# Kernel optimization log

Measured on AMD Instinct MI355X. Metric: run time of the kernel, lower is better.

## Reference

```python
import jax, jax.numpy as jnp
import numpy as np

HOP_NUM = 3
N_NODES = 40000
N_EDGES = 640000
IN_DIM = 128
N_ALPHAS = HOP_NUM * (HOP_NUM + 1) // 2  # triangular layerRegular params


def setup_inputs() -> dict:
    key = jax.random.key(0)
    k_h, k_d, k_a, k_s, k_t = jax.random.split(key, 5)
    h = jax.random.normal(k_h, (N_NODES, IN_DIM), dtype=jnp.float32)
    d = jax.random.uniform(k_d, (N_NODES,), dtype=jnp.float32)  # degree normalization per node
    alphas = jax.random.uniform(k_a, (N_ALPHAS,), dtype=jnp.float32)
    src = jax.random.randint(k_s, (N_EDGES,), 0, N_NODES, dtype=jnp.int32)
    dst = jax.random.randint(k_t, (N_EDGES,), 0, N_NODES, dtype=jnp.int32)
    return {"h": h, "d": d, "alphas": alphas, "src": src, "dst": dst}


def reference(h, d, alphas, src, dst):
    n = h.shape[0]
    # edge_applying: e = 1 * d[dst] * d[src]  (symmetric-normalized edge weight)
    e = d[dst] * d[src]                      # [E]
    outs = [h]
    k = 0
    for i in range(HOP_NUM):
        feat = h
        for q in range(i + 1):
            # update_all(u_mul_e('h','e'), sum): agg[v] = sum_{(u,v)} feat[u] * e
            msg = feat[src] * e[:, None]     # [E, D]
            agg = jax.ops.segment_sum(msg, dst, num_segments=n)  # [N, D]
            a = alphas[k]; k += 1
            feat = agg * a + (1.0 - a) * feat
            # feature_drop with p=0.0 (eval) is identity
        outs.append(feat)
    return jnp.concatenate(outs, axis=1)       # [N, (HOP_NUM+1)*D]
```

## Files before the change

kernel.cpp:

```cpp
#include <hip/hip_runtime.h>


#define NN  40000
#define NE  640000
#define CAP 64

__device__ inline unsigned short f2h(float f) {
    _Float16 h = (_Float16)f;
    return *(unsigned short*)&h;
}
__device__ inline float h2f(unsigned short u) {
    _Float16 h = *(_Float16*)&u;
    return (float)h;
}
__device__ inline unsigned short f2bf(float f) {
    unsigned int x = __float_as_uint(f);
    x += 0x7fffu + ((x >> 16) & 1u);
    return (unsigned short)(x >> 16);
}
__device__ inline unsigned int pack_bf2(float x, float y) {
    return ((unsigned int)f2bf(y) << 16) | (unsigned int)f2bf(x);
}
__device__ inline float bflo(unsigned int u) { return __uint_as_float(u << 16); }
__device__ inline float bfhi(unsigned int u) { return __uint_as_float(u & 0xffff0000u); }

__global__ __launch_bounds__(256) void build_cvt_k(
    const int* __restrict__ src, const int* __restrict__ dst,
    const float* __restrict__ deg, const float* __restrict__ h,
    int* __restrict__ counts, unsigned int* __restrict__ buck,
    unsigned int* __restrict__ hb) {
    int b = blockIdx.x;
    if (b < NE / 256) {
        int e = b * 256 + threadIdx.x;
        int s = src[e];
        int v = dst[e];
        int slot = atomicAdd(&counts[v], 1);
        if (slot < CAP) {
            float w = deg[s] * deg[v];
            buck[v * CAP + slot] = ((unsigned int)f2h(w) << 16) | (unsigned int)s;
        }
    } else {
        int i = (b - NE / 256) * 256 + threadIdx.x;
        if (i < NN * 64) {
            float2 f = *(const float2*)(h + (size_t)i * 2);
            hb[i] = pack_bf2(f.x, f.y);
        }
    }
}

__device__ inline float2 gather_node(
    const unsigned int* __restrict__ feat,
    const int* __restrict__ counts, const unsigned int* __restrict__ buck,
    int v, int lane) {
    int vs = __builtin_amdgcn_readfirstlane(v);
    int cnt = counts[vs];
    if (cnt > CAP) cnt = CAP;
    const unsigned int* brow = buck + (size_t)vs * CAP;

    float ax = 0.f, ay = 0.f, bx = 0.f, by = 0.f;
    float cx = 0.f, cy = 0.f, dx = 0.f, dy = 0.f;
    for (int j = 0; j < cnt; j += 8) {
        unsigned int uu[8];
#pragma unroll
        for (int k = 0; k < 8; ++k) uu[k] = brow[j + k];
        float wj[8]; int sj[8];
#pragma unroll
        for (int k = 0; k < 8; ++k) {
            bool ok = (j + k) < cnt;
            wj[k] = ok ? h2f((unsigned short)(uu[k] >> 16)) : 0.f;
            sj[k] = ok ? (int)(uu[k] & 0xffffu) : 0;
        }
        unsigned int fj[8];
#pragma unroll
        for (int k = 0; k < 8; ++k)
            fj[k] = feat[(size_t)sj[k] * 64 + lane];
#pragma unroll
        for (int k = 0; k < 8; k += 4) {
            ax = fmaf(wj[k + 0], bflo(fj[k + 0]), ax);
            ay = fmaf(wj[k + 0], bfhi(fj[k + 0]), ay);
            bx = fmaf(wj[k + 1], bflo(fj[k + 1]), bx);
            by = fmaf(wj[k + 1], bfhi(fj[k + 1]), by);
            cx = fmaf(wj[k + 2], bflo(fj[k + 2]), cx);
            cy = fmaf(wj[k + 2], bfhi(fj[k + 2]), cy);
            dx = fmaf(wj[k + 3], bflo(fj[k + 3]), dx);
            dy = fmaf(wj[k + 3], bfhi(fj[k + 3]), dy);
        }
    }
    return make_float2((ax + bx) + (cx + dx), (ay + by) + (cy + dy));
}

__global__ __launch_bounds__(256) void agg_k(
    const unsigned int* __restrict__ feat,
    const int* __restrict__ counts, const unsigned int* __restrict__ buck,
    unsigned int* __restrict__ outf) {
    int gid  = blockIdx.x * 256 + threadIdx.x;
    int v    = gid >> 6;
    int lane = gid & 63;
    if (v >= NN) return;
    float2 acc = gather_node(feat, counts, buck, v, lane);
    outf[(size_t)v * 64 + lane] = pack_bf2(acc.x, acc.y);
}

__global__ __launch_bounds__(256) void agg3_fused_k(
    const unsigned int* __restrict__ p2b,
    const float* __restrict__ h,
    const unsigned int* __restrict__ p1b,
    const int* __restrict__ counts, const unsigned int* __restrict__ buck,
    const float* __restrict__ alphas, float* __restrict__ out) {
    int gid  = blockIdx.x * 256 + threadIdx.x;
    int v    = gid >> 6;
    int lane = gid & 63;
    if (v >= NN) return;
    float2 p3 = gather_node(p2b, counts, buck, v, lane);

    float a0 = alphas[0], a1 = alphas[1], a2 = alphas[2];
    float a3 = alphas[3], a4 = alphas[4], a5 = alphas[5];
    float c1p = a0, c1h = 1.f - a0;
    float c2pp = a2 * a1;
    float c2p  = a2 * (1.f - a1) + (1.f - a2) * a1;
    float c2h  = (1.f - a2) * (1.f - a1);
    float s2pp = a4 * a3;
    float s2p  = a4 * (1.f - a3) + (1.f - a4) * a3;
    float s2h  = (1.f - a4) * (1.f - a3);
    float c3ppp = a5 * s2pp;
    float c3pp  = a5 * s2p + (1.f - a5) * s2pp;
    float c3p   = a5 * s2h + (1.f - a5) * s2p;
    float c3h   = (1.f - a5) * s2h;

    int i2 = lane * 2;
    float2 hf = *(const float2*)(h + (size_t)v * 128 + i2);
    unsigned int u1 = p1b[(size_t)v * 64 + lane];
    unsigned int u2 = p2b[(size_t)v * 64 + lane];
    float q1x = bflo(u1), q1y = bfhi(u1);
    float q2x = bflo(u2), q2y = bfhi(u2);

    float2 r1, r2, r3;
    r1.x = c1p * q1x + c1h * hf.x;
    r1.y = c1p * q1y + c1h * hf.y;
    r2.x = c2pp * q2x + c2p * q1x + c2h * hf.x;
    r2.y = c2pp * q2y + c2p * q1y + c2h * hf.y;
    r3.x = c3ppp * p3.x + c3pp * q2x + c3p * q1x + c3h * hf.x;
    r3.y = c3ppp * p3.y + c3pp * q2y + c3p * q1y + c3h * hf.y;

    float* o = out + (size_t)v * 512;
    *(float2*)(o + i2)       = hf;
    *(float2*)(o + 128 + i2) = r1;
    *(float2*)(o + 256 + i2) = r2;
    *(float2*)(o + 384 + i2) = r3;
}

extern "C" void kernel_launch(void* const* d_in, const int* in_sizes, int n_in,
                              void* d_out, int out_size, void* d_ws, size_t ws_size,
                              hipStream_t stream) {
    const float* h      = (const float*)d_in[0];
    const float* deg    = (const float*)d_in[1];
    const float* alphas = (const float*)d_in[2];
    const int*   src    = (const int*)d_in[3];
    const int*   dst    = (const int*)d_in[4];
    float* out = (float*)d_out;

    char* ws = (char*)d_ws;
    int*          counts = (int*)(ws + 0);
    unsigned int* buck   = (unsigned int*)(ws + 160000);
    unsigned int* hb     = (unsigned int*)(ws + 10400000);
    unsigned int* p1b    = (unsigned int*)(ws + 20640000);
    unsigned int* p2b    = (unsigned int*)(ws + 30880000);

    hipMemsetAsync(counts, 0, NN * sizeof(int), stream);
    build_cvt_k<<<NE / 256 + (NN * 64 + 255) / 256, 256, 0, stream>>>(
        src, dst, deg, h, counts, buck, hb);

    agg_k<<<NN / 4, 256, 0, stream>>>(hb,  counts, buck, p1b);
    agg_k<<<NN / 4, 256, 0, stream>>>(p1b, counts, buck, p2b);
    agg3_fused_k<<<NN / 4, 256, 0, stream>>>(p2b, h, p1b, counts, buck,
                                             alphas, out);
}
```

Measured before the change: 212.4 us.

## Merge all stages into one cooperative persistent kernel with grid syncs

Replaces the memset and the four separate launches (bucket build plus bf16 conversion, two aggregation hops, and the fused final hop) with one cooperative kernel of 1024 blocks. Grid-stride loops cover each phase, and grid.sync() separates them. The aim is to remove launch gaps and per-kernel tail effects. The cost is grid-wide barrier overhead, lower occupancy than a full launch (launch bounds 256,4), and a fixed grid that must stay co-resident for the cooperative launch to succeed.

Result: slower. 663.4 us (+212.4%).

```diff
diff --git a/kernel.cpp b/kernel.cpp
--- a/kernel.cpp
+++ b/kernel.cpp
@@ -1,76 +1,58 @@
 #include <hip/hip_runtime.h>
+#include <hip/hip_cooperative_groups.h>
 
+
+namespace cg = cooperative_groups;
 
 #define NN  40000
 #define NE  640000
 #define CAP 64
 
-__device__ inline unsigned short f2h(float f) {
+typedef unsigned int uint;
+typedef unsigned short ushort;
+
+__device__ inline ushort f2h(float f) {
     _Float16 h = (_Float16)f;
-    return *(unsigned short*)&h;
+    return *(ushort*)&h;
 }
-__device__ inline float h2f(unsigned short u) {
+__device__ inline float h2f(ushort u) {
     _Float16 h = *(_Float16*)&u;
     return (float)h;
 }
-__device__ inline unsigned short f2bf(float f) {
-    unsigned int x = __float_as_uint(f);
+__device__ inline ushort f2bf(float f) {
+    uint x = __float_as_uint(f);
     x += 0x7fffu + ((x >> 16) & 1u);
-    return (unsigned short)(x >> 16);
+    return (ushort)(x >> 16);
 }
-__device__ inline unsigned int pack_bf2(float x, float y) {
-    return ((unsigned int)f2bf(y) << 16) | (unsigned int)f2bf(x);
+__device__ inline uint pack_bf2(float x, float y) {
+    return ((uint)f2bf(y) << 16) | (uint)f2bf(x);
 }
-__device__ inline float bflo(unsigned int u) { return __uint_as_float(u << 16); }
-__device__ inline float bfhi(unsigned int u) { return __uint_as_float(u & 0xffff0000u); }
-
-__global__ __launch_bounds__(256) void build_cvt_k(
-    const int* __restrict__ src, const int* __restrict__ dst,
-    const float* __restrict__ deg, const float* __restrict__ h,
-    int* __restrict__ counts, unsigned int* __restrict__ buck,
-    unsigned int* __restrict__ hb) {
-    int b = blockIdx.x;
-    if (b < NE / 256) {
-        int e = b * 256 + threadIdx.x;
-        int s = src[e];
-        int v = dst[e];
-        int slot = atomicAdd(&counts[v], 1);
-        if (slot < CAP) {
-            float w = deg[s] * deg[v];
-            buck[v * CAP + slot] = ((unsigned int)f2h(w) << 16) | (unsigned int)s;
-        }
-    } else {
-        int i = (b - NE / 256) * 256 + threadIdx.x;
-        if (i < NN * 64) {
-            float2 f = *(const float2*)(h + (size_t)i * 2);
-            hb[i] = pack_bf2(f.x, f.y);
-        }
-    }
-}
+__device__ inline float bflo(uint u) { return __uint_as_float(u << 16); }
+__device__ inline float bfhi(uint u) { return __uint_as_float(u & 0xffff0000u); }
 
 __device__ inline float2 gather_node(
-    const unsigned int* __restrict__ feat,
-    const int* __restrict__ counts, const unsigned int* __restrict__ buck,
+    const uint* __restrict__ feat,
+    const int* __restrict__ counts, const uint* __restrict__ buck,
     int v, int lane) {
     int vs = __builtin_amdgcn_readfirstlane(v);
     int cnt = counts[vs];
     if (cnt > CAP) cnt = CAP;
-    const unsigned int* brow = buck + (size_t)vs * CAP;
+    const uint* brow = buck + (size_t)vs * CAP;
 
     float ax = 0.f, ay = 0.f, bx = 0.f, by = 0.f;
     float cx = 0.f, cy = 0.f, dx = 0.f, dy = 0.f;
     for (int j = 0; j < cnt; j += 8) {
-        unsigned int uu[8];
+        uint uu[8];
 #pragma unroll
         for (int k = 0; k < 8; ++k) uu[k] = brow[j + k];
         float wj[8]; int sj[8];
 #pragma unroll
         for (int k = 0; k < 8; ++k) {
             bool ok = (j + k) < cnt;
-            wj[k] = ok ? h2f((unsigned short)(uu[k] >> 16)) : 0.f;
+            wj[k] = ok ? h2f((ushort)(uu[k] >> 16)) : 0.f;
             sj[k] = ok ? (int)(uu[k] & 0xffffu) : 0;
         }
-        unsigned int fj[8];
+        uint fj[8];
 #pragma unroll
         for (int k = 0; k < 8; ++k)
             fj[k] = feat[(size_t)sj[k] * 64 + lane];
@@ -89,29 +71,49 @@
     return make_float2((ax + bx) + (cx + dx), (ay + by) + (cy + dy));
 }
 
-__global__ __launch_bounds__(256) void agg_k(
-    const unsigned int* __restrict__ feat,
-    const int* __restrict__ counts, const unsigned int* __restrict__ buck,
-    unsigned int* __restrict__ outf) {
-    int gid  = blockIdx.x * 256 + threadIdx.x;
-    int v    = gid >> 6;
-    int lane = gid & 63;
-    if (v >= NN) return;
-    float2 acc = gather_node(feat, counts, buck, v, lane);
-    outf[(size_t)v * 64 + lane] = pack_bf2(acc.x, acc.y);
-}
+__global__ __launch_bounds__(256, 4) void mega_k(
+    const float* __restrict__ h, const float* __restrict__ deg,
+    const float* __restrict__ alphas,
+    const int* __restrict__ src, const int* __restrict__ dst,
+    int* __restrict__ counts, uint* __restrict__ buck,
+    uint* __restrict__ hb, uint* __restrict__ p1b, uint* __restrict__ p2b,
+    float* __restrict__ out) {
+    cg::grid_group grid = cg::this_grid();
+    const int nthr = (int)(gridDim.x * 256);
+    const int tid  = (int)(blockIdx.x * 256 + threadIdx.x);
+    const int lane = tid & 63;
+    const int wid  = tid >> 6;
+    const int wstr = nthr >> 6;
 
-__global__ __launch_bounds__(256) void agg3_fused_k(
-    const unsigned int* __restrict__ p2b,
-    const float* __restrict__ h,
-    const unsigned int* __restrict__ p1b,
-    const int* __restrict__ counts, const unsigned int* __restrict__ buck,
-    const float* __restrict__ alphas, float* __restrict__ out) {
-    int gid  = blockIdx.x * 256 + threadIdx.x;
-    int v    = gid >> 6;
-    int lane = gid & 63;
-    if (v >= NN) return;
-    float2 p3 = gather_node(p2b, counts, buck, v, lane);
+    for (int i = tid; i < NN; i += nthr) counts[i] = 0;
+    grid.sync();
+
+    for (int e = tid; e < NE; e += nthr) {
+        int s = src[e];
+        int v = dst[e];
+        int slot = atomicAdd(&counts[v], 1);
+        if (slot < CAP) {
+            float w = deg[s] * deg[v];
+            buck[v * CAP + slot] = ((uint)f2h(w) << 16) | (uint)s;
+        }
+    }
+    for (int i = tid; i < NN * 64; i += nthr) {
+        float2 f = *(const float2*)(h + (size_t)i * 2);
+        hb[i] = pack_bf2(f.x, f.y);
+    }
+    grid.sync();
+
+    for (int v = wid; v < NN; v += wstr) {
+        float2 a = gather_node(hb, counts, buck, v, lane);
+        p1b[(size_t)v * 64 + lane] = pack_bf2(a.x, a.y);
+    }
+    grid.sync();
+
+    for (int v = wid; v < NN; v += wstr) {
+        float2 a = gather_node(p1b, counts, buck, v, lane);
+        p2b[(size_t)v * 64 + lane] = pack_bf2(a.x, a.y);
+    }
+    grid.sync();
 
     float a0 = alphas[0], a1 = alphas[1], a2 = alphas[2];
     float a3 = alphas[3], a4 = alphas[4], a5 = alphas[5];
@@ -127,26 +129,29 @@
     float c3p   = a5 * s2h + (1.f - a5) * s2p;
     float c3h   = (1.f - a5) * s2h;
 
-    int i2 = lane * 2;
-    float2 hf = *(const float2*)(h + (size_t)v * 128 + i2);
-    unsigned int u1 = p1b[(size_t)v * 64 + lane];
-    unsigned int u2 = p2b[(size_t)v * 64 + lane];
-    float q1x = bflo(u1), q1y = bfhi(u1);
-    float q2x = bflo(u2), q2y = bfhi(u2);
+    for (int v = wid; v < NN; v += wstr) {
+        float2 p3 = gather_node(p2b, counts, buck, v, lane);
+        int i2 = lane * 2;
+        float2 hf = *(const float2*)(h + (size_t)v * 128 + i2);
+        uint u1 = p1b[(size_t)v * 64 + lane];
+        uint u2 = p2b[(size_t)v * 64 + lane];
+        float q1x = bflo(u1), q1y = bfhi(u1);
+        float q2x = bflo(u2), q2y = bfhi(u2);
 
-    float2 r1, r2, r3;
-    r1.x = c1p * q1x + c1h * hf.x;
-    r1.y = c1p * q1y + c1h * hf.y;
-    r2.x = c2pp * q2x + c2p * q1x + c2h * hf.x;
-    r2.y = c2pp * q2y + c2p * q1y + c2h * hf.y;
-    r3.x = c3ppp * p3.x + c3pp * q2x + c3p * q1x + c3h * hf.x;
-    r3.y = c3ppp * p3.y + c3pp * q2y + c3p * q1y + c3h * hf.y;
+        float2 r1, r2, r3;
+        r1.x = c1p * q1x + c1h * hf.x;
+        r1.y = c1p * q1y + c1h * hf.y;
+        r2.x = c2pp * q2x + c2p * q1x + c2h * hf.x;
+        r2.y = c2pp * q2y + c2p * q1y + c2h * hf.y;
+        r3.x = c3ppp * p3.x + c3pp * q2x + c3p * q1x + c3h * hf.x;
+        r3.y = c3ppp * p3.y + c3pp * q2y + c3p * q1y + c3h * hf.y;
 
-    float* o = out + (size_t)v * 512;
-    *(float2*)(o + i2)       = hf;
-    *(float2*)(o + 128 + i2) = r1;
-    *(float2*)(o + 256 + i2) = r2;
-    *(float2*)(o + 384 + i2) = r3;
+        float* o = out + (size_t)v * 512;
+        *(float2*)(o + i2)       = hf;
+        *(float2*)(o + 128 + i2) = r1;
+        *(float2*)(o + 256 + i2) = r2;
+        *(float2*)(o + 384 + i2) = r3;
+    }
 }
 
 extern "C" void kernel_launch(void* const* d_in, const int* in_sizes, int n_in,
@@ -160,18 +165,17 @@
     float* out = (float*)d_out;
 
     char* ws = (char*)d_ws;
-    int*          counts = (int*)(ws + 0);
-    unsigned int* buck   = (unsigned int*)(ws + 160000);
-    unsigned int* hb     = (unsigned int*)(ws + 10400000);
-    unsigned int* p1b    = (unsigned int*)(ws + 20640000);
-    unsigned int* p2b    = (unsigned int*)(ws + 30880000);
+    int*  counts = (int*)(ws + 0);
+    uint* buck   = (uint*)(ws + 160000);
+    uint* hb     = (uint*)(ws + 10400000);
+    uint* p1b    = (uint*)(ws + 20640000);
+    uint* p2b    = (uint*)(ws + 30880000);
 
-    hipMemsetAsync(counts, 0, NN * sizeof(int), stream);
-    build_cvt_k<<<NE / 256 + (NN * 64 + 255) / 256, 256, 0, stream>>>(
-        src, dst, deg, h, counts, buck, hb);
-
-    agg_k<<<NN / 4, 256, 0, stream>>>(hb,  counts, buck, p1b);
-    agg_k<<<NN / 4, 256, 0, stream>>>(p1b, counts, buck, p2b);
-    agg3_fused_k<<<NN / 4, 256, 0, stream>>>(p2b, h, p1b, counts, buck,
-                                             alphas, out);
+    void* args[] = {
+        (void*)&h, (void*)&deg, (void*)&alphas, (void*)&src, (void*)&dst,
+        (void*)&counts, (void*)&buck, (void*)&hb, (void*)&p1b, (void*)&p2b,
+        (void*)&out
+    };
+    (void)hipLaunchCooperativeKernel((const void*)mega_k, dim3(1024),
+                                     dim3(256), args, 0, stream);
 }
```
